# Kernel tuning notes

Measured on AMD Instinct MI355X. Metric: run time of the kernel, lower is better.

## Reference

```python
import jax, jax.numpy as jnp
import numpy as np

SEQ = 8          # sequence_size
C = 128          # in_channels / factor (hidden + input channels)
BN_EPS = 1e-5


def setup_inputs() -> dict:
    key = jax.random.key(0)
    k1, k2 = jax.random.split(key)
    x = jax.random.normal(k1, (32, C, 64, 64), dtype=jnp.float32)          # (B*T, C, H, W)
    w_conv = jax.random.normal(k2, (4 * C, 2 * C, 3, 3), dtype=jnp.float32) * 0.05  # OIHW
    b_conv = jnp.zeros((4 * C,), dtype=jnp.float32)
    gamma = jnp.ones((C,), dtype=jnp.float32)
    beta = jnp.zeros((C,), dtype=jnp.float32)
    run_mean = jnp.zeros((C,), dtype=jnp.float32)
    run_var = jnp.ones((C,), dtype=jnp.float32)
    return {"x": x, "w_conv": w_conv, "b_conv": b_conv, "gamma": gamma,
            "beta": beta, "run_mean": run_mean, "run_var": run_var}


def _convlstm_scan(x_seq, w_conv, b_conv):
    # x_seq: (B, T, C, H, W); zero initial (h, c) states (reset path)
    B, T, Cc, H, W = x_seq.shape
    h0 = jnp.zeros((B, Cc, H, W), x_seq.dtype)
    c0 = jnp.zeros((B, Cc, H, W), x_seq.dtype)

    def step(carry, x_t):
        h, c = carry
        z = jax.lax.conv_general_dilated(
            jnp.concatenate([x_t, h], axis=1), w_conv,
            window_strides=(1, 1), padding='SAME',
            dimension_numbers=('NCHW', 'OIHW', 'NCHW'))
        z = z + b_conv[None, :, None, None]
        i, f, o, g = jnp.split(z, 4, axis=1)
        c_next = jax.nn.sigmoid(f) * c + jax.nn.sigmoid(i) * jnp.tanh(g)
        h_next = jax.nn.sigmoid(o) * jnp.tanh(c_next)
        return (h_next, c_next), h_next

    _, hs = jax.lax.scan(step, (h0, c0), jnp.swapaxes(x_seq, 0, 1))  # hs: (T, B, C, H, W)
    return jnp.swapaxes(hs, 0, 1)  # (B, T, C, H, W)


def reference(x, w_conv, b_conv, gamma, beta, run_mean, run_var):
    BT, Cc, H, W = x.shape
    x_seq = x.reshape(BT // SEQ, SEQ, Cc, H, W)
    hs = _convlstm_scan(x_seq, w_conv, b_conv)           # (B, T, C, H, W)
    out = hs.reshape(-1, Cc, H, W)                        # (B*T, C, H, W)
    # BatchNorm2d (eval mode: running stats) + ReLU
    inv = jax.lax.rsqrt(run_var + BN_EPS)
    out = (out - run_mean[None, :, None, None]) * (inv * gamma)[None, :, None, None] \
          + beta[None, :, None, None]
    return jax.nn.relu(out)
```

## Files before the change

### kernel.cpp

```cpp
#include <hip/hip_runtime.h>
#include <hip/hip_bf16.h>
#include <math.h>

typedef __attribute__((ext_vector_type(8))) short bf16x8;
typedef __attribute__((ext_vector_type(4))) float f32x4;

#define FRAME_PAD (66*66*128)

#define GLOAD_LDS16(g, l) \
    __builtin_amdgcn_global_load_lds((const __attribute__((address_space(1))) void*)(g), \
                                     (__attribute__((address_space(3))) void*)(l), 16, 0, 0)

#define WAITV6    asm volatile("s_waitcnt vmcnt(6)" ::: "memory")
#define WAITV0    asm volatile("s_waitcnt vmcnt(0)" ::: "memory")
#define WAITLGKM0 asm volatile("s_waitcnt lgkmcnt(0)" ::: "memory")
#define SBAR      __builtin_amdgcn_s_barrier()

__device__ __forceinline__ float sigmoidf_(float x) { return 1.0f / (1.0f + __expf(-x)); }
__device__ __forceinline__ float tanhf_(float x) {
    x = fminf(fmaxf(x, -15.0f), 15.0f);
    float e = __expf(2.0f * x);
    return (e - 1.0f) / (e + 1.0f);
}
__device__ __forceinline__ float b2f_(short u) {
    unsigned int v = ((unsigned int)(unsigned short)u) << 16;
    return __builtin_bit_cast(float, v);
}
__device__ __forceinline__ short f2b_(float f) {
    __hip_bfloat16 hb = __float2bfloat16(f);
    return *reinterpret_cast<short*>(&hb);
}

__global__ void wt_kernel(const float* __restrict__ w, __hip_bfloat16* __restrict__ wt)
{
    int idx = blockIdx.x * 256 + threadIdx.x;
    if (idx >= 9 * 512 * 256) return;
    int ic  = idx & 255;
    int n   = (idx >> 8) & 511;
    int tap = idx >> 17;
    int c = n >> 2, g = n & 3;
    int oc = g * 128 + c;
    wt[idx] = __float2bfloat16(w[((size_t)oc * 256 + (size_t)ic) * 9 + tap]);
}

__global__ void border_kernel(__hip_bfloat16* __restrict__ x_pad,
                              __hip_bfloat16* __restrict__ h_pad)
{
    const int fr = blockIdx.x;
    __hip_bfloat16* base = (fr < 32) ? x_pad + (size_t)fr * FRAME_PAD
                                     : h_pad + (size_t)(fr - 32) * FRAME_PAD;
    bf16x8 z = {};
    for (int u = threadIdx.x; u < 2112; u += 256) {
        int half = (u >= 1056) ? 1 : 0;
        int v = u - half * 1056;
        *(bf16x8*)(base + (size_t)(half * 65 * 66) * 128 + (size_t)v * 8) = z;
    }
    for (int u = threadIdx.x; u < 2048; u += 256) {
        int yy = 1 + (u >> 5);
        int r = u & 31;
        int side = r >> 4, c16 = r & 15;
        *(bf16x8*)(base + (size_t)(yy * 66 + side * 65) * 128 + (size_t)c16 * 8) = z;
    }
}

__global__ void xpose_kernel(const float* __restrict__ x, __hip_bfloat16* __restrict__ x_pad)
{
    __shared__ float tile[64][129];
    const int f = blockIdx.x >> 6;
    const int y = blockIdx.x & 63;
    const int tid = threadIdx.x;
    const float* src = x + (size_t)f * 524288 + (size_t)y * 64;
    #pragma unroll
    for (int it = 0; it < 8; ++it) {
        int c  = it * 16 + (tid >> 4);
        int xq = tid & 15;
        float4 v = *(const float4*)(src + (size_t)c * 4096 + xq * 4);
        tile[xq * 4 + 0][c] = v.x;
        tile[xq * 4 + 1][c] = v.y;
        tile[xq * 4 + 2][c] = v.z;
        tile[xq * 4 + 3][c] = v.w;
    }
    __syncthreads();
    __hip_bfloat16* dst = x_pad + (size_t)f * FRAME_PAD + (size_t)((y + 1) * 66 + 1) * 128;
    const int g = tid & 15;
    #pragma unroll
    for (int it = 0; it < 4; ++it) {
        int xr = it * 16 + (tid >> 4);
        bf16x8 o;
        #pragma unroll
        for (int e = 0; e < 8; ++e) o[e] = f2b_(tile[xr][g * 8 + e]);
        *(bf16x8*)(dst + (size_t)xr * 128 + g * 8) = o;
    }
}

template<bool T0>
__global__ __launch_bounds__(512, 2)
void conv_gemm(const __hip_bfloat16* __restrict__ x_pad,
               const __hip_bfloat16* __restrict__ h_pad,
               const __hip_bfloat16* __restrict__ wt,
               const float* __restrict__ bias,
               float* __restrict__ c_state, int t)
{
    __shared__ alignas(16) __hip_bfloat16 S_s[3][256 * 64];
    __shared__ alignas(16) __hip_bfloat16 W_s[2][128 * 64];
    const int tid  = threadIdx.x;
    const int wv   = tid >> 6;
    const int lane = tid & 63;
    const int KT   = T0 ? 18 : 36;

    const int F    = blockIdx.x;
    const int tile = (F >> 3) + (F & 7) * 32;
    const int n0   = (tile & 3) * 128;
    const int mblk = tile >> 2;
    const int b    = mblk >> 4;
    const int y0   = (mblk & 15) * 4;
    const int m0   = mblk * 256;

    const __hip_bfloat16* xf = x_pad + (size_t)(b * 8 + t) * FRAME_PAD;
    const __hip_bfloat16* hf = h_pad + (size_t)(b * 8 + (T0 ? 0 : t - 1)) * FRAME_PAD;

    int aOff[4], bOff[2];
    #pragma unroll
    for (int j = 0; j < 4; ++j) {
        int sid = j * 512 + tid;
        int row = sid >> 3;
        int q   = (sid & 7) ^ (row & 7);
        aOff[j] = ((y0 + (row >> 6)) * 66 + (row & 63)) * 128 + q * 8;
    }
    #pragma unroll
    for (int j = 0; j < 2; ++j) {
        int sid = j * 512 + tid;
        int row = sid >> 3;
        int q   = (sid & 7) ^ (row & 7);
        bOff[j] = (n0 + row) * 256 + q * 8;
    }

    auto stageA = [&](__hip_bfloat16* Sl, int kt, int j0, int j1) {
        int tap, icq;
        const __hip_bfloat16* sb;
        if constexpr (T0) { tap = kt >> 1; icq = (kt & 1) * 64; sb = xf + icq; }
        else { tap = kt >> 2; icq = (kt & 3) * 64;
               sb = (icq < 128) ? (xf + icq) : (hf + (icq - 128)); }
        const int dy = tap / 3, dx = tap % 3;
        const __hip_bfloat16* a = sb + (dy * 66 + dx) * 128;
        for (int j = j0; j < j1; ++j)
            GLOAD_LDS16(a + aOff[j], Sl + (size_t)(j * 512 + tid) * 8);
    };
    auto stageW = [&](__hip_bfloat16* Wl, int kt) {
        int tap, icq;
        if constexpr (T0) { tap = kt >> 1; icq = (kt & 1) * 64; }
        else { tap = kt >> 2; icq = (kt & 3) * 64; }
        const __hip_bfloat16* bsrc = wt + tap * 131072 + icq;
        #pragma unroll
        for (int j = 0; j < 2; ++j)
            GLOAD_LDS16(bsrc + bOff[j], Wl + (size_t)(j * 512 + tid) * 8);
    };

    const int wm = wv >> 1, wn = wv & 1;
    const int fr = lane & 15, fq = lane >> 4;
    const int slot = (fq ^ (fr & 7)) * 8;
    const int sOff0 = (wm * 64 + fr) * 64 + slot, sOff1 = sOff0 ^ 32;
    const int wOff0 = (wn * 64 + fr) * 64 + slot, wOff1 = wOff0 ^ 32;

    f32x4 acc[4][4] = {};

    __hip_bfloat16 *Sr = &S_s[0][0], *Sn = &S_s[1][0], *Sf = &S_s[2][0];
    __hip_bfloat16 *Wr = &W_s[0][0], *Wn = &W_s[1][0];

    stageA(Sr, 0, 0, 4); stageW(Wr, 0);
    stageA(Sn, 1, 0, 4); stageW(Wn, 1);
    WAITV6;
    SBAR;

    #pragma unroll 1
    for (int kt = 0; kt < KT; ++kt) {
        bf16x8 w0[4], w1[4], s0[4], s1[4];
        #pragma unroll
        for (int ri = 0; ri < 4; ++ri) w0[ri] = *(const bf16x8*)(Wr + wOff0 + ri * 1024);
        #pragma unroll
        for (int ci = 0; ci < 4; ++ci) s0[ci] = *(const bf16x8*)(Sr + sOff0 + ci * 1024);
        #pragma unroll
        for (int ri = 0; ri < 4; ++ri) w1[ri] = *(const bf16x8*)(Wr + wOff1 + ri * 1024);
        if (kt < KT - 2) stageA(Sf, kt + 2, 0, 2);
        SBAR;
        WAITLGKM0;
        __builtin_amdgcn_s_setprio(1);
        #pragma unroll
        for (int ri = 0; ri < 4; ++ri)
            #pragma unroll
            for (int ci = 0; ci < 4; ++ci)
                acc[ri][ci] = __builtin_amdgcn_mfma_f32_16x16x32_bf16(w0[ri], s0[ci], acc[ri][ci], 0, 0, 0);
        __builtin_amdgcn_s_setprio(0);
        SBAR;
        #pragma unroll
        for (int ci = 0; ci < 4; ++ci) s1[ci] = *(const bf16x8*)(Sr + sOff1 + ci * 1024);
        if (kt < KT - 2) { stageA(Sf, kt + 2, 2, 4); stageW(Wr, kt + 2); }
        SBAR;
        WAITLGKM0;
        __builtin_amdgcn_s_setprio(1);
        #pragma unroll
        for (int ri = 0; ri < 4; ++ri)
            #pragma unroll
            for (int ci = 0; ci < 4; ++ci)
                acc[ri][ci] = __builtin_amdgcn_mfma_f32_16x16x32_bf16(w1[ri], s1[ci], acc[ri][ci], 0, 0, 0);
        __builtin_amdgcn_s_setprio(0);
        if (kt < KT - 2) { WAITV6; } else { WAITV0; }
        SBAR;
        __hip_bfloat16* tp = Sr; Sr = Sn; Sn = Sf; Sf = tp;
        __hip_bfloat16* tw = Wr; Wr = Wn; Wn = tw;
    }

    const int c0    = (n0 >> 2) + wn * 16;
    const int mcol0 = m0 + wm * 64 + fr;
    __hip_bfloat16* hout = (__hip_bfloat16*)h_pad + (size_t)(b * 8 + t) * FRAME_PAD;
    #pragma unroll
    for (int ri = 0; ri < 4; ++ri) {
        const int c = c0 + ri * 4 + fq;
        const float bi  = bias[c];
        const float bfv = bias[128 + c];
        const float bo  = bias[256 + c];
        const float bg  = bias[384 + c];
        float* csrow = c_state + (size_t)c * 16384;
        #pragma unroll
        for (int ci = 0; ci < 4; ++ci) {
            const int m = mcol0 + ci * 16;
            const int s = m & 4095;
            const float cold = T0 ? 0.0f : csrow[m];
            const float zi = acc[ri][ci][0] + bi;
            const float zf = acc[ri][ci][1] + bfv;
            const float zo = acc[ri][ci][2] + bo;
            const float zg = acc[ri][ci][3] + bg;
            const float cn = sigmoidf_(zf) * cold + sigmoidf_(zi) * tanhf_(zg);
            const float h  = sigmoidf_(zo) * tanhf_(cn);
            csrow[m] = cn;
            hout[(size_t)(((s >> 6) + 1) * 66 + (s & 63) + 1) * 128 + c] = __float2bfloat16(h);
        }
    }
}

__global__ void bn_out_kernel(const __hip_bfloat16* __restrict__ h_pad,
                              const float* __restrict__ gamma, const float* __restrict__ beta,
                              const float* __restrict__ rmean, const float* __restrict__ rvar,
                              float* __restrict__ out)
{
    __shared__ float tile[64][129];
    __shared__ float sc_s[128], sh_s[128];
    const int fo  = blockIdx.x >> 6;
    const int y   = blockIdx.x & 63;
    const int tid = threadIdx.x;
    if (tid < 128) {
        float sc = gamma[tid] * rsqrtf(rvar[tid] + 1e-5f);
        sc_s[tid] = sc;
        sh_s[tid] = beta[tid] - rmean[tid] * sc;
    }
    __syncthreads();
    const __hip_bfloat16* src =
        h_pad + (size_t)fo * FRAME_PAD + (size_t)((y + 1) * 66 + 1) * 128;
    const int g = tid & 15;
    float sc[8], sh[8];
    #pragma unroll
    for (int e = 0; e < 8; ++e) { sc[e] = sc_s[g * 8 + e]; sh[e] = sh_s[g * 8 + e]; }
    #pragma unroll
    for (int it = 0; it < 4; ++it) {
        int xr = it * 16 + (tid >> 4);
        bf16x8 v = *(const bf16x8*)(src + (size_t)xr * 128 + g * 8);
        #pragma unroll
        for (int e = 0; e < 8; ++e)
            tile[xr][g * 8 + e] = fmaxf(b2f_(v[e]) * sc[e] + sh[e], 0.0f);
    }
    __syncthreads();
    float* dst = out + (size_t)fo * 524288 + (size_t)y * 64;
    #pragma unroll
    for (int it = 0; it < 8; ++it) {
        int c  = it * 16 + (tid >> 4);
        int xq = tid & 15;
        float4 o;
        o.x = tile[xq * 4 + 0][c];
        o.y = tile[xq * 4 + 1][c];
        o.z = tile[xq * 4 + 2][c];
        o.w = tile[xq * 4 + 3][c];
        *(float4*)(dst + (size_t)c * 4096 + xq * 4) = o;
    }
}

extern "C" void kernel_launch(void* const* d_in, const int* in_sizes, int n_in,
                              void* d_out, int out_size, void* d_ws, size_t ws_size,
                              hipStream_t stream)
{
    const float* x      = (const float*)d_in[0];
    const float* w_conv = (const float*)d_in[1];
    const float* b_conv = (const float*)d_in[2];
    const float* gamma  = (const float*)d_in[3];
    const float* beta   = (const float*)d_in[4];
    const float* rmean  = (const float*)d_in[5];
    const float* rvar   = (const float*)d_in[6];
    float* out = (float*)d_out;

    if (ws_size < 82116608u) return;

    char* ws = (char*)d_ws;
    __hip_bfloat16* Wt    = (__hip_bfloat16*)(ws);
    __hip_bfloat16* x_pad = (__hip_bfloat16*)(ws + 2359296);
    __hip_bfloat16* h_pad = (__hip_bfloat16*)(ws + 38043648);
    float* c_state        = (float*)(ws + 73728000);

    wt_kernel<<<4608, 256, 0, stream>>>(w_conv, Wt);
    xpose_kernel<<<2048, 256, 0, stream>>>(x, x_pad);
    border_kernel<<<64, 256, 0, stream>>>(x_pad, h_pad);

    conv_gemm<true><<<256, 512, 0, stream>>>(x_pad, h_pad, Wt, b_conv, c_state, 0);
    for (int t = 1; t < 8; ++t)
        conv_gemm<false><<<256, 512, 0, stream>>>(x_pad, h_pad, Wt, b_conv, c_state, t);

    bn_out_kernel<<<2048, 256, 0, stream>>>(h_pad, gamma, beta, rmean, rvar, out);
}
```

Before: 382.1 us.

## Triple-buffer weight tiles and cut GEMM main loop to one barrier

Weight tiles in LDS go from double to triple buffering, matching the activation tiles, so each stage can be prefetched two k-steps ahead in one batch. The main loop now has a single wait-plus-barrier at the top instead of four barriers, and all fragment reads are issued together before both MFMA halves. This is meant to cut synchronisation stalls per k-step. In exchange it uses more LDS and no longer interleaves prefetch issue with the two MFMA halves, which can raise register pressure and expose load latency differently.

```diff
diff --git a/kernel.cpp b/kernel.cpp
--- a/kernel.cpp
+++ b/kernel.cpp
@@ -13,8 +13,8 @@
 
 #define WAITV6    asm volatile("s_waitcnt vmcnt(6)" ::: "memory")
 #define WAITV0    asm volatile("s_waitcnt vmcnt(0)" ::: "memory")
-#define WAITLGKM0 asm volatile("s_waitcnt lgkmcnt(0)" ::: "memory")
 #define SBAR      __builtin_amdgcn_s_barrier()
+#define MEMPIN    asm volatile("" ::: "memory")
 
 __device__ __forceinline__ float sigmoidf_(float x) { return 1.0f / (1.0f + __expf(-x)); }
 __device__ __forceinline__ float tanhf_(float x) {
@@ -102,7 +102,7 @@
                float* __restrict__ c_state, int t)
 {
     __shared__ alignas(16) __hip_bfloat16 S_s[3][256 * 64];
-    __shared__ alignas(16) __hip_bfloat16 W_s[2][128 * 64];
+    __shared__ alignas(16) __hip_bfloat16 W_s[3][128 * 64];
     const int tid  = threadIdx.x;
     const int wv   = tid >> 6;
     const int lane = tid & 63;
@@ -135,7 +135,7 @@
         bOff[j] = (n0 + row) * 256 + q * 8;
     }
 
-    auto stageA = [&](__hip_bfloat16* Sl, int kt, int j0, int j1) {
+    auto STAGE = [&](__hip_bfloat16* Sl, __hip_bfloat16* Wl, int kt) {
         int tap, icq;
         const __hip_bfloat16* sb;
         if constexpr (T0) { tap = kt >> 1; icq = (kt & 1) * 64; sb = xf + icq; }
@@ -143,13 +143,9 @@
                sb = (icq < 128) ? (xf + icq) : (hf + (icq - 128)); }
         const int dy = tap / 3, dx = tap % 3;
         const __hip_bfloat16* a = sb + (dy * 66 + dx) * 128;
-        for (int j = j0; j < j1; ++j)
+        #pragma unroll
+        for (int j = 0; j < 4; ++j)
             GLOAD_LDS16(a + aOff[j], Sl + (size_t)(j * 512 + tid) * 8);
-    };
-    auto stageW = [&](__hip_bfloat16* Wl, int kt) {
-        int tap, icq;
-        if constexpr (T0) { tap = kt >> 1; icq = (kt & 1) * 64; }
-        else { tap = kt >> 2; icq = (kt & 3) * 64; }
         const __hip_bfloat16* bsrc = wt + tap * 131072 + icq;
         #pragma unroll
         for (int j = 0; j < 2; ++j)
@@ -165,49 +161,44 @@
     f32x4 acc[4][4] = {};
 
     __hip_bfloat16 *Sr = &S_s[0][0], *Sn = &S_s[1][0], *Sf = &S_s[2][0];
-    __hip_bfloat16 *Wr = &W_s[0][0], *Wn = &W_s[1][0];
-
-    stageA(Sr, 0, 0, 4); stageW(Wr, 0);
-    stageA(Sn, 1, 0, 4); stageW(Wn, 1);
-    WAITV6;
-    SBAR;
+    __hip_bfloat16 *Wr = &W_s[0][0], *Wn = &W_s[1][0], *Wf = &W_s[2][0];
+
+    STAGE(Sr, Wr, 0);
+    STAGE(Sn, Wn, 1);
 
     #pragma unroll 1
     for (int kt = 0; kt < KT; ++kt) {
+        if (kt < KT - 1) { WAITV6; } else { WAITV0; }
+        SBAR;
+        MEMPIN;
+        if (kt < KT - 2) STAGE(Sf, Wf, kt + 2);
+
         bf16x8 w0[4], w1[4], s0[4], s1[4];
         #pragma unroll
-        for (int ri = 0; ri < 4; ++ri) w0[ri] = *(const bf16x8*)(Wr + wOff0 + ri * 1024);
-        #pragma unroll
-        for (int ci = 0; ci < 4; ++ci) s0[ci] = *(const bf16x8*)(Sr + sOff0 + ci * 1024);
-        #pragma unroll
-        for (int ri = 0; ri < 4; ++ri) w1[ri] = *(const bf16x8*)(Wr + wOff1 + ri * 1024);
-        if (kt < KT - 2) stageA(Sf, kt + 2, 0, 2);
-        SBAR;
-        WAITLGKM0;
+        for (int ri = 0; ri < 4; ++ri) {
+            w0[ri] = *(const bf16x8*)(Wr + wOff0 + ri * 1024);
+            w1[ri] = *(const bf16x8*)(Wr + wOff1 + ri * 1024);
+        }
+        #pragma unroll
+        for (int ci = 0; ci < 4; ++ci) {
+            s0[ci] = *(const bf16x8*)(Sr + sOff0 + ci * 1024);
+            s1[ci] = *(const bf16x8*)(Sr + sOff1 + ci * 1024);
+        }
         __builtin_amdgcn_s_setprio(1);
         #pragma unroll
         for (int ri = 0; ri < 4; ++ri)
             #pragma unroll
             for (int ci = 0; ci < 4; ++ci)
                 acc[ri][ci] = __builtin_amdgcn_mfma_f32_16x16x32_bf16(w0[ri], s0[ci], acc[ri][ci], 0, 0, 0);
-        __builtin_amdgcn_s_setprio(0);
-        SBAR;
-        #pragma unroll
-        for (int ci = 0; ci < 4; ++ci) s1[ci] = *(const bf16x8*)(Sr + sOff1 + ci * 1024);
-        if (kt < KT - 2) { stageA(Sf, kt + 2, 2, 4); stageW(Wr, kt + 2); }
-        SBAR;
-        WAITLGKM0;
-        __builtin_amdgcn_s_setprio(1);
         #pragma unroll
         for (int ri = 0; ri < 4; ++ri)
             #pragma unroll
             for (int ci = 0; ci < 4; ++ci)
                 acc[ri][ci] = __builtin_amdgcn_mfma_f32_16x16x32_bf16(w1[ri], s1[ci], acc[ri][ci], 0, 0, 0);
         __builtin_amdgcn_s_setprio(0);
-        if (kt < KT - 2) { WAITV6; } else { WAITV0; }
-        SBAR;
+
         __hip_bfloat16* tp = Sr; Sr = Sn; Sn = Sf; Sf = tp;
-        __hip_bfloat16* tw = Wr; Wr = Wn; Wn = tw;
+        __hip_bfloat16* tw = Wr; Wr = Wn; Wn = Wf; Wf = tw;
     }
 
     const int c0    = (n0 >> 2) + wn * 16;
```

Measured after the change: 424.6 us. 11.1% more time.
